# Optimization experiments

Hardware: AMD Instinct MI355X
Metric: run time of the kernel (lower is better)

Reference implementation:

```python
import jax, jax.numpy as jnp
import numpy as np

B, CIN, COUT, H, W, WDIM = 16, 256, 256, 64, 64, 512


def setup_inputs() -> dict:
    key = jax.random.key(0)
    ks = jax.random.split(key, 4)
    return {
        "x": jax.random.normal(ks[0], (B, CIN, H, W), dtype=jnp.float32),
        "w": jax.random.normal(ks[1], (B, WDIM), dtype=jnp.float32),
        "affine_w": jax.random.normal(ks[2], (CIN, WDIM), dtype=jnp.float32),
        "affine_b": jnp.ones((CIN,), dtype=jnp.float32),
        "weight": jax.random.normal(ks[3], (COUT, CIN, 1, 1), dtype=jnp.float32),
        "bias": jnp.zeros((COUT,), dtype=jnp.float32),
    }


def reference(x, w, affine_w, affine_b, weight, bias):
    # Affine: FullyConnectedLayer with weight_gain = 1/sqrt(w_dim), bias_init=1
    wg = 1.0 / np.sqrt(WDIM).astype(np.float32)
    styles = w @ (affine_w.T * wg) + affine_b  # [B, CIN]

    # Pre-normalize weight and styles (demodulate branch)
    wk = weight[:, :, 0, 0]  # [COUT, CIN] (1x1 kernel)
    wk = wk * jax.lax.rsqrt(jnp.mean(jnp.square(weight), axis=(1, 2, 3)))[:, None]
    s = styles * jax.lax.rsqrt(jnp.mean(jnp.square(styles)))  # [B, CIN]

    # Per-sample modulated weights: [B, COUT, CIN]
    wb = wk[None, :, :] * s[:, None, :]
    dcoef = jax.lax.rsqrt(jnp.sum(jnp.square(wb), axis=2) + 1e-8)  # [B, COUT]
    wb = wb * dcoef[:, :, None]

    # Grouped 1x1 conv == batched GEMM over spatial positions
    y = jnp.einsum('bihw,boi->bohw', x, wb) + bias[None, :, None, None]

    # Bilinear upsample x2 (align_corners=False == half-pixel, jax default)
    y = jax.image.resize(y, (B, COUT, 2 * H, 2 * W), method='bilinear')
    return y
```

## Files before the change

### kernel.cpp

```cpp
#include <hip/hip_runtime.h>
#include <hip/hip_bf16.h>

#define B_   16
#define CIN  256
#define COUT 256
#define HH   64
#define WW   64
#define WDIM 512
#define OH   128
#define OW   128

#define PX   128
#define LDK  264
#define YLP  136
#define MCH  32

typedef __attribute__((ext_vector_type(8))) short short8;
typedef __attribute__((ext_vector_type(4))) float f32x4;

__device__ __forceinline__ unsigned short f2bf(float f) {
    __hip_bfloat16 h = __float2bfloat16(f);
    return *reinterpret_cast<unsigned short*>(&h);
}
__device__ __forceinline__ float bf2f(unsigned short u) {
    unsigned int t = ((unsigned int)u) << 16;
    return *reinterpret_cast<float*>(&t);
}


__global__ __launch_bounds__(256) void k_styles(const float* __restrict__ w,
                                                const float* __restrict__ aw,
                                                const float* __restrict__ ab,
                                                float* __restrict__ ws) {
    int b = blockIdx.x, i = threadIdx.x;
    const float4* wr = (const float4*)(w + b * WDIM);
    const float4* ar = (const float4*)(aw + (size_t)i * WDIM);
    float acc = 0.f;
    #pragma unroll 4
    for (int k = 0; k < WDIM / 4; ++k) {
        float4 wv = wr[k], av = ar[k];
        acc += wv.x * av.x + wv.y * av.y + wv.z * av.z + wv.w * av.w;
    }
    const float wg = 0.04419417382415922f;
    float st = acc * wg + ab[i];
    ws[64 + b * CIN + i] = st;
    __shared__ float sred[256];
    sred[i] = st * st;
    __syncthreads();
    for (int s = 128; s > 0; s >>= 1) {
        if (i < s) sred[i] += sred[i + s];
        __syncthreads();
    }
    if (i == 0) ws[b] = sred[0];
}

__global__ __launch_bounds__(64) void k_wb(const float* __restrict__ weight,
                                           const float* __restrict__ ws,
                                           unsigned short* __restrict__ wb) {
    int o = blockIdx.x, b = blockIdx.y, l = threadIdx.x;
    float tot = 0.f;
    #pragma unroll
    for (int j = 0; j < B_; ++j) tot += ws[j];
    float srs = rsqrtf(tot / (float)(B_ * CIN));
    float4 wk = *(const float4*)(weight + (size_t)o * CIN + l * 4);
    float ss = wk.x * wk.x + wk.y * wk.y + wk.z * wk.z + wk.w * wk.w;
    #pragma unroll
    for (int off = 32; off; off >>= 1) ss += __shfl_xor(ss, off);
    float wkn = rsqrtf(ss / (float)CIN);
    float4 st = *(const float4*)(ws + 64 + b * CIN + l * 4);
    float4 t;
    t.x = wk.x * wkn * st.x * srs;
    t.y = wk.y * wkn * st.y * srs;
    t.z = wk.z * wkn * st.z * srs;
    t.w = wk.w * wkn * st.w * srs;
    float s2 = t.x * t.x + t.y * t.y + t.z * t.z + t.w * t.w;
    #pragma unroll
    for (int off = 32; off; off >>= 1) s2 += __shfl_xor(s2, off);
    float dcoef = rsqrtf(s2 + 1e-8f);
    ushort4 pk;
    pk.x = f2bf(t.x * dcoef);
    pk.y = f2bf(t.y * dcoef);
    pk.z = f2bf(t.z * dcoef);
    pk.w = f2bf(t.w * dcoef);
    *(ushort4*)(wb + ((size_t)b * COUT + o) * CIN + l * 4) = pk;
}

__global__ __launch_bounds__(512, 4) void k_main(const float* __restrict__ x,
                                                 const float* __restrict__ bias,
                                                 const unsigned short* __restrict__ wb,
                                                 float* __restrict__ out) {
    __shared__ __align__(16) unsigned short xt[PX * LDK];
    __shared__ __align__(16) unsigned short ylds[MCH * YLP];
    const int r = blockIdx.x;
    const int b = blockIdx.y;
    const int tid = threadIdx.x;
    const int lane = tid & 63;

    {
        const int g = tid & 31;
        const int kk = tid >> 5;
        const int row = g >> 4;
        const int col4 = (g & 15) * 4;
        const int grow = min(r + row, HH - 1);
        const float* xp = x + (size_t)b * CIN * HH * WW + grow * WW + col4;
        const int px0 = g * 4;
        #pragma unroll
        for (int grp = 0; grp < 2; ++grp) {
            float4 v[8];
            #pragma unroll
            for (int c = 0; c < 8; ++c)
                v[c] = *(const float4*)(xp + (size_t)(kk * 16 + grp * 8 + c) * (HH * WW));
            #pragma unroll
            for (int j = 0; j < 4; ++j) {
                union { short8 s; unsigned short u[8]; } pk;
                #pragma unroll
                for (int c = 0; c < 8; ++c) {
                    float f = (j == 0) ? v[c].x : (j == 1) ? v[c].y : (j == 2) ? v[c].z : v[c].w;
                    pk.u[c] = f2bf(f);
                }
                *reinterpret_cast<short8*>(&xt[(px0 + j) * LDK + kk * 16 + grp * 8]) = pk.s;
            }
        }
    }
    __syncthreads();

    const int wv = tid >> 6;
    const int wm = wv & 1, wn = wv >> 1;
    const int n0 = wn * 32;
    const int hi = lane >> 4, lo = lane & 15;
    const unsigned short* wbp = wb + (size_t)b * COUT * CIN;

    const int ostart = (r == 0) ? 0 : (2 * r + 1);
    const int oend = (r == HH - 1) ? OH : (2 * r + 3);
    const int nrows = oend - ostart;
    const int iters = 2 * nrows;

    for (int mc = 0; mc < COUT / MCH; ++mc) {
        const int m0 = mc * MCH + wm * 16;
        f32x4 acc0 = {0.f, 0.f, 0.f, 0.f};
        f32x4 acc1 = {0.f, 0.f, 0.f, 0.f};
        #pragma unroll
        for (int ks = 0; ks < 8; ++ks) {
            const int k0 = ks * 32;
            short8 a  = *(const short8*)(wbp + (size_t)(m0 + lo) * CIN + k0 + hi * 8);
            short8 b0 = *(const short8*)&xt[(n0 + lo) * LDK + k0 + hi * 8];
            short8 b1 = *(const short8*)&xt[(n0 + 16 + lo) * LDK + k0 + hi * 8];
            acc0 = __builtin_amdgcn_mfma_f32_16x16x32_bf16(a, b0, acc0, 0, 0, 0);
            acc1 = __builtin_amdgcn_mfma_f32_16x16x32_bf16(a, b1, acc1, 0, 0, 0);
        }
        const int mloc = wm * 16 + hi * 4;
        #pragma unroll
        for (int j = 0; j < 4; ++j) {
            float bs = bias[mc * MCH + mloc + j];
            ylds[(mloc + j) * YLP + n0 + lo]      = f2bf(acc0[j] + bs);
            ylds[(mloc + j) * YLP + n0 + 16 + lo] = f2bf(acc1[j] + bs);
        }
        __syncthreads();

        for (int it = 0; it < iters; ++it) {
            int f = it * 512 + tid;
            int q = f & 31;
            int ch = (f >> 5) & 31;
            int ori = f >> 10;
            int o = ostart + ori;
            int yr0 = (o - 1) >> 1;
            int lr0 = min(max(yr0, 0), HH - 1) - r;
            int lr1 = min(yr0 + 1, HH - 1) - r;
            float wr0 = (o & 1) ? 0.75f : 0.25f;
            float wr1 = 1.f - wr0;
            int cA = max(2 * q - 1, 0), cB = 2 * q;
            int cC = min(2 * q + 1, WW - 1), cD = min(2 * q + 2, WW - 1);
            const unsigned short* Y = &ylds[ch * YLP];
            float rA = wr0 * bf2f(Y[lr0 * 64 + cA]) + wr1 * bf2f(Y[lr1 * 64 + cA]);
            float rB = wr0 * bf2f(Y[lr0 * 64 + cB]) + wr1 * bf2f(Y[lr1 * 64 + cB]);
            float rC = wr0 * bf2f(Y[lr0 * 64 + cC]) + wr1 * bf2f(Y[lr1 * 64 + cC]);
            float rD = wr0 * bf2f(Y[lr0 * 64 + cD]) + wr1 * bf2f(Y[lr1 * 64 + cD]);
            float4 ov;
            ov.x = 0.25f * rA + 0.75f * rB;
            ov.y = 0.75f * rB + 0.25f * rC;
            ov.z = 0.25f * rB + 0.75f * rC;
            ov.w = 0.75f * rC + 0.25f * rD;
            float* op = out + ((((size_t)b * COUT + mc * MCH + ch) * OH + o) * OW + q * 4);
            *(float4*)op = ov;
        }
        __syncthreads();
    }
}

extern "C" void kernel_launch(void* const* d_in, const int* in_sizes, int n_in,
                              void* d_out, int out_size, void* d_ws, size_t ws_size,
                              hipStream_t stream) {
    (void)in_sizes; (void)n_in; (void)out_size; (void)ws_size;
    const float* x      = (const float*)d_in[0];
    const float* w      = (const float*)d_in[1];
    const float* aw     = (const float*)d_in[2];
    const float* ab     = (const float*)d_in[3];
    const float* weight = (const float*)d_in[4];
    const float* bias   = (const float*)d_in[5];
    float* out = (float*)d_out;
    float* wsf = (float*)d_ws;
    unsigned short* wb = (unsigned short*)((char*)d_ws + 32768);

    hipLaunchKernelGGL(k_styles, dim3(16), dim3(256), 0, stream, w, aw, ab, wsf);
    hipLaunchKernelGGL(k_wb, dim3(COUT, B_), dim3(64), 0, stream, weight, wsf, wb);
    hipLaunchKernelGGL(k_main, dim3(HH, B_), dim3(512), 0, stream, x, bias, wb, out);
}
```

Before: 122.9 us.

## Split fused conv+upsample into conv kernel writing bf16 intermediate and separate upsample kernel

The fused kernel, which recomputed a two-row GEMM tile (one row redundant) per block, is split in two. A conv kernel computes exactly one input row per block and writes bf16 y to workspace. A separate upsample kernel reads three bf16 rows per output pair and uses lane shuffles for horizontal neighbours. This removes the doubled GEMM and staging work and lets each kernel tune its own occupancy, at the cost of an extra global round trip for the bf16 intermediate (about 32MB write plus reads) and an extra launch.

Measured after the change: 152.1 us. 1.24x slower.

```diff
diff --git a/kernel.cpp b/kernel.cpp
--- a/kernel.cpp
+++ b/kernel.cpp
@@ -10,9 +10,8 @@
 #define OH   128
 #define OW   128
 
-#define PX   128
 #define LDK  264
-#define YLP  136
+#define YLP  72
 #define MCH  32
 
 typedef __attribute__((ext_vector_type(8))) short short8;
@@ -85,11 +84,11 @@
     *(ushort4*)(wb + ((size_t)b * COUT + o) * CIN + l * 4) = pk;
 }
 
-__global__ __launch_bounds__(512, 4) void k_main(const float* __restrict__ x,
+__global__ __launch_bounds__(512, 6) void k_conv(const float* __restrict__ x,
                                                  const float* __restrict__ bias,
                                                  const unsigned short* __restrict__ wb,
-                                                 float* __restrict__ out) {
-    __shared__ __align__(16) unsigned short xt[PX * LDK];
+                                                 unsigned short* __restrict__ y) {
+    __shared__ __align__(16) unsigned short xt[WW * LDK];
     __shared__ __align__(16) unsigned short ylds[MCH * YLP];
     const int r = blockIdx.x;
     const int b = blockIdx.y;
@@ -97,94 +96,99 @@
     const int lane = tid & 63;
 
     {
-        const int g = tid & 31;
-        const int kk = tid >> 5;
-        const int row = g >> 4;
-        const int col4 = (g & 15) * 4;
-        const int grow = min(r + row, HH - 1);
-        const float* xp = x + (size_t)b * CIN * HH * WW + grow * WW + col4;
-        const int px0 = g * 4;
-        #pragma unroll
-        for (int grp = 0; grp < 2; ++grp) {
-            float4 v[8];
+        const int g = tid & 15;
+        const int kk = tid >> 4;
+        const float* xp = x + (size_t)b * CIN * HH * WW + r * WW + g * 4;
+        float4 v[8];
+        #pragma unroll
+        for (int c = 0; c < 8; ++c)
+            v[c] = *(const float4*)(xp + (size_t)(kk * 8 + c) * (HH * WW));
+        #pragma unroll
+        for (int j = 0; j < 4; ++j) {
+            union { short8 s; unsigned short u[8]; } pk;
             #pragma unroll
-            for (int c = 0; c < 8; ++c)
-                v[c] = *(const float4*)(xp + (size_t)(kk * 16 + grp * 8 + c) * (HH * WW));
-            #pragma unroll
-            for (int j = 0; j < 4; ++j) {
-                union { short8 s; unsigned short u[8]; } pk;
-                #pragma unroll
-                for (int c = 0; c < 8; ++c) {
-                    float f = (j == 0) ? v[c].x : (j == 1) ? v[c].y : (j == 2) ? v[c].z : v[c].w;
-                    pk.u[c] = f2bf(f);
-                }
-                *reinterpret_cast<short8*>(&xt[(px0 + j) * LDK + kk * 16 + grp * 8]) = pk.s;
+            for (int c = 0; c < 8; ++c) {
+                float f = (j == 0) ? v[c].x : (j == 1) ? v[c].y : (j == 2) ? v[c].z : v[c].w;
+                pk.u[c] = f2bf(f);
             }
+            *reinterpret_cast<short8*>(&xt[(g * 4 + j) * LDK + kk * 8]) = pk.s;
         }
     }
     __syncthreads();
 
     const int wv = tid >> 6;
     const int wm = wv & 1, wn = wv >> 1;
-    const int n0 = wn * 32;
+    const int n0 = wn * 16;
     const int hi = lane >> 4, lo = lane & 15;
     const unsigned short* wbp = wb + (size_t)b * COUT * CIN;
 
-    const int ostart = (r == 0) ? 0 : (2 * r + 1);
-    const int oend = (r == HH - 1) ? OH : (2 * r + 3);
-    const int nrows = oend - ostart;
-    const int iters = 2 * nrows;
-
     for (int mc = 0; mc < COUT / MCH; ++mc) {
         const int m0 = mc * MCH + wm * 16;
-        f32x4 acc0 = {0.f, 0.f, 0.f, 0.f};
-        f32x4 acc1 = {0.f, 0.f, 0.f, 0.f};
+        f32x4 acc = {0.f, 0.f, 0.f, 0.f};
         #pragma unroll
         for (int ks = 0; ks < 8; ++ks) {
             const int k0 = ks * 32;
-            short8 a  = *(const short8*)(wbp + (size_t)(m0 + lo) * CIN + k0 + hi * 8);
-            short8 b0 = *(const short8*)&xt[(n0 + lo) * LDK + k0 + hi * 8];
-            short8 b1 = *(const short8*)&xt[(n0 + 16 + lo) * LDK + k0 + hi * 8];
-            acc0 = __builtin_amdgcn_mfma_f32_16x16x32_bf16(a, b0, acc0, 0, 0, 0);
-            acc1 = __builtin_amdgcn_mfma_f32_16x16x32_bf16(a, b1, acc1, 0, 0, 0);
+            short8 a = *(const short8*)(wbp + (size_t)(m0 + lo) * CIN + k0 + hi * 8);
+            short8 bx = *(const short8*)&xt[(n0 + lo) * LDK + k0 + hi * 8];
+            acc = __builtin_amdgcn_mfma_f32_16x16x32_bf16(a, bx, acc, 0, 0, 0);
         }
         const int mloc = wm * 16 + hi * 4;
         #pragma unroll
         for (int j = 0; j < 4; ++j) {
             float bs = bias[mc * MCH + mloc + j];
-            ylds[(mloc + j) * YLP + n0 + lo]      = f2bf(acc0[j] + bs);
-            ylds[(mloc + j) * YLP + n0 + 16 + lo] = f2bf(acc1[j] + bs);
+            ylds[(mloc + j) * YLP + n0 + lo] = f2bf(acc[j] + bs);
         }
         __syncthreads();
-
-        for (int it = 0; it < iters; ++it) {
-            int f = it * 512 + tid;
-            int q = f & 31;
-            int ch = (f >> 5) & 31;
-            int ori = f >> 10;
-            int o = ostart + ori;
-            int yr0 = (o - 1) >> 1;
-            int lr0 = min(max(yr0, 0), HH - 1) - r;
-            int lr1 = min(yr0 + 1, HH - 1) - r;
-            float wr0 = (o & 1) ? 0.75f : 0.25f;
-            float wr1 = 1.f - wr0;
-            int cA = max(2 * q - 1, 0), cB = 2 * q;
-            int cC = min(2 * q + 1, WW - 1), cD = min(2 * q + 2, WW - 1);
-            const unsigned short* Y = &ylds[ch * YLP];
-            float rA = wr0 * bf2f(Y[lr0 * 64 + cA]) + wr1 * bf2f(Y[lr1 * 64 + cA]);
-            float rB = wr0 * bf2f(Y[lr0 * 64 + cB]) + wr1 * bf2f(Y[lr1 * 64 + cB]);
-            float rC = wr0 * bf2f(Y[lr0 * 64 + cC]) + wr1 * bf2f(Y[lr1 * 64 + cC]);
-            float rD = wr0 * bf2f(Y[lr0 * 64 + cD]) + wr1 * bf2f(Y[lr1 * 64 + cD]);
-            float4 ov;
-            ov.x = 0.25f * rA + 0.75f * rB;
-            ov.y = 0.75f * rB + 0.25f * rC;
-            ov.z = 0.25f * rB + 0.75f * rC;
-            ov.w = 0.75f * rC + 0.25f * rD;
-            float* op = out + ((((size_t)b * COUT + mc * MCH + ch) * OH + o) * OW + q * 4);
-            *(float4*)op = ov;
+        {
+            const int ch = tid >> 4, sub = tid & 15;
+            ushort4 v4 = *(const ushort4*)&ylds[ch * YLP + sub * 4];
+            *(ushort4*)(y + ((size_t)(b * COUT + mc * MCH + ch) * (HH * WW)) + r * WW + sub * 4) = v4;
         }
         __syncthreads();
     }
+}
+
+__global__ __launch_bounds__(256, 8) void k_up(const unsigned short* __restrict__ y,
+                                               float* __restrict__ out) {
+    const int tid = threadIdx.x;
+    const int t = tid & 31;
+    const int s = tid >> 5;
+    const int idx = blockIdx.x * 8 + s;
+    const int p = idx & 63;
+    const int ch = (idx >> 6) & 255;
+    const int b = idx >> 14;
+
+    const unsigned short* yb = y + (size_t)(b * COUT + ch) * (HH * WW);
+    const int pm1 = max(p - 1, 0), pp1 = min(p + 1, HH - 1);
+    unsigned int T = *(const unsigned int*)(yb + pm1 * WW + 2 * t);
+    unsigned int M = *(const unsigned int*)(yb + p   * WW + 2 * t);
+    unsigned int Bt = *(const unsigned int*)(yb + pp1 * WW + 2 * t);
+
+    float tB = bf2f((unsigned short)(T & 0xffff)), tC = bf2f((unsigned short)(T >> 16));
+    float mB = bf2f((unsigned short)(M & 0xffff)), mC = bf2f((unsigned short)(M >> 16));
+    float bB = bf2f((unsigned short)(Bt & 0xffff)), bC = bf2f((unsigned short)(Bt >> 16));
+
+    float aB = 0.25f * tB + 0.75f * mB, aC = 0.25f * tC + 0.75f * mC;
+    float eB = 0.75f * mB + 0.25f * bB, eC = 0.75f * mC + 0.25f * bC;
+
+    float aA = __shfl_up(aC, 1, 32);  if (t == 0)  aA = aB;
+    float aD = __shfl_down(aB, 1, 32); if (t == 31) aD = aC;
+    float eA = __shfl_up(eC, 1, 32);  if (t == 0)  eA = eB;
+    float eD = __shfl_down(eB, 1, 32); if (t == 31) eD = eC;
+
+    float4 o0, o1;
+    o0.x = 0.25f * aA + 0.75f * aB;
+    o0.y = 0.75f * aB + 0.25f * aC;
+    o0.z = 0.25f * aB + 0.75f * aC;
+    o0.w = 0.75f * aC + 0.25f * aD;
+    o1.x = 0.25f * eA + 0.75f * eB;
+    o1.y = 0.75f * eB + 0.25f * eC;
+    o1.z = 0.25f * eB + 0.75f * eC;
+    o1.w = 0.75f * eC + 0.25f * eD;
+
+    float* op = out + (size_t)(b * COUT + ch) * (OH * OW) + (2 * p) * OW + 4 * t;
+    *(float4*)op = o0;
+    *(float4*)(op + OW) = o1;
 }
 
 extern "C" void kernel_launch(void* const* d_in, const int* in_sizes, int n_in,
@@ -200,8 +204,10 @@
     float* out = (float*)d_out;
     float* wsf = (float*)d_ws;
     unsigned short* wb = (unsigned short*)((char*)d_ws + 32768);
+    unsigned short* y  = (unsigned short*)((char*)d_ws + (4u << 20));
 
     hipLaunchKernelGGL(k_styles, dim3(16), dim3(256), 0, stream, w, aw, ab, wsf);
     hipLaunchKernelGGL(k_wb, dim3(COUT, B_), dim3(64), 0, stream, weight, wsf, wb);
-    hipLaunchKernelGGL(k_main, dim3(HH, B_), dim3(512), 0, stream, x, bias, wb, out);
-}
+    hipLaunchKernelGGL(k_conv, dim3(HH, B_), dim3(512), 0, stream, x, bias, wb, y);
+    hipLaunchKernelGGL(k_up, dim3(B_ * COUT * HH / 8), dim3(256), 0, stream, y, out);
+}
```
